# Kernel tuning notes

Measured on AMD Instinct MI355X. Metric: run time of the kernel, lower is better.

The kernel has to match this reference:

```python
import jax, jax.numpy as jnp
import numpy as np

HEADS = 16
EPS = 1e-6


def _rmsnorm(x, gamma):
    # x: [..., head_dim]
    inv = jax.lax.rsqrt(jnp.mean(x * x, axis=-1, keepdims=True) + EPS)
    return x * inv * gamma


def setup_inputs() -> dict:
    key = jax.random.key(0)
    ks = jax.random.split(key, 7)
    B, L, Lc, D, CTX = 4, 4096, 1024, 1024, 1024
    hd = D // HEADS
    s = 1.0 / np.sqrt(D)
    return {
        "x": jax.random.normal(ks[0], (B, L, D), jnp.float32),
        "ctx": jax.random.normal(ks[1], (B, Lc, CTX), jnp.float32),
        "Wq": jax.random.normal(ks[2], (D, D), jnp.float32) * s,
        "Wkv": jax.random.normal(ks[3], (CTX, 2 * D), jnp.float32) * s,
        "Wproj": jax.random.normal(ks[4], (D, D), jnp.float32) * s,
        "q_gamma": jnp.ones((hd,), jnp.float32),
        "k_gamma": jnp.ones((hd,), jnp.float32),
    }


def reference(x, ctx, Wq, Wkv, Wproj, q_gamma, k_gamma):
    B, L, D = x.shape
    Lc = ctx.shape[1]
    H = HEADS
    hd = D // H
    # projections
    q = (x @ Wq).reshape(B, L, H, hd).transpose(0, 2, 1, 3)        # [B,H,L,hd]
    kv = (ctx @ Wkv).reshape(B, Lc, 2, H, hd).transpose(2, 0, 3, 1, 4)
    k, v = kv[0], kv[1]                                            # [B,H,Lc,hd]
    # per-head QK RMSNorm
    q = _rmsnorm(q, q_gamma)
    k = _rmsnorm(k, k_gamma)
    scale = 1.0 / np.sqrt(hd)
    attn = jnp.einsum("bhld,bhmd->bhlm", q, k) * scale             # [B,H,L,Lc]
    attn = jax.nn.softmax(attn, axis=-1)
    out = jnp.einsum("bhlm,bhmd->bhld", attn, v)                   # [B,H,L,hd]
    out = out.transpose(0, 2, 1, 3).reshape(B, L, D)
    return out @ Wproj
```

## Files before the change

### kernel.cpp

```cpp
#include <hip/hip_runtime.h>

typedef __bf16 bf16x8 __attribute__((ext_vector_type(8)));
typedef __bf16 bf16x4 __attribute__((ext_vector_type(4)));
typedef float f32x4 __attribute__((ext_vector_type(4)));

__device__ __forceinline__ void gl_lds16(const void* g, void* l) {
  __builtin_amdgcn_global_load_lds(
      (const __attribute__((address_space(1))) unsigned int*)g,
      (__attribute__((address_space(3))) unsigned int*)l, 16, 0, 0);
}

__global__ __launch_bounds__(256) void conv_bf16_kernel(
    const float* __restrict__ in, __bf16* __restrict__ out, int n4) {
  int i = blockIdx.x * 256 + threadIdx.x;
  if (i < n4) {
    float4 v = ((const float4*)in)[i];
    bf16x4 o;
    o[0] = (__bf16)v.x; o[1] = (__bf16)v.y; o[2] = (__bf16)v.z; o[3] = (__bf16)v.w;
    *(bf16x4*)(out + (size_t)i * 4) = o;
  }
}

__global__ __launch_bounds__(256) void tconv_kernel(
    const float* __restrict__ W, __bf16* __restrict__ Wt, int R, int C) {
  __shared__ float t[32][33];
  int c0 = blockIdx.x * 32, r0 = blockIdx.y * 32;
  int tx = threadIdx.x, ty = threadIdx.y;
#pragma unroll
  for (int i = 0; i < 4; ++i)
    t[ty + i * 8][tx] = W[(size_t)(r0 + ty + i * 8) * C + c0 + tx];
  __syncthreads();
#pragma unroll
  for (int i = 0; i < 4; ++i)
    Wt[(size_t)(c0 + ty + i * 8) * R + r0 + tx] = (__bf16)t[tx][ty + i * 8];
}

template <int NORM, int OUTF32>
__global__ __launch_bounds__(256) void gemm_kernel(
    const __bf16* __restrict__ A, const __bf16* __restrict__ Bt,
    void* __restrict__ Cout, void* __restrict__ Cout2,
    int M, int N, int K, const float* __restrict__ gamma) {
  __shared__ alignas(16) __bf16 Alds[2][128 * 32];
  __shared__ alignas(16) __bf16 Blds[2][128 * 32];
  const int tid = threadIdx.x;
  const int w = tid >> 6, l = tid & 63;
  const int lg = l & 15, lh = l >> 4;
  const int wr = w >> 1, wc = w & 1;

  const int nbx = gridDim.x;
  const int lid = blockIdx.y * nbx + blockIdx.x;
  const int cpx = (nbx * gridDim.y) >> 3;
  const int swz = (lid & 7) * cpx + (lid >> 3);
  const int brow = (swz / nbx) * 128, bcol = (swz % nbx) * 128;

  const f32x4 zero = {0.f, 0.f, 0.f, 0.f};
  f32x4 acc[4][4];
#pragma unroll
  for (int m = 0; m < 4; ++m)
#pragma unroll
    for (int n = 0; n < 4; ++n) acc[m][n] = zero;

  auto STAGE = [&](int buf, int k0) {
#pragma unroll
    for (int j = 0; j < 2; ++j) {
      int c = j * 256 + w * 64 + l;
      gl_lds16(A + (size_t)(brow + (c >> 2)) * K + k0 + (c & 3) * 8,
               (char*)Alds[buf] + (j * 256 + w * 64) * 16);
      gl_lds16(Bt + (size_t)(bcol + (c >> 2)) * K + k0 + (c & 3) * 8,
               (char*)Blds[buf] + (j * 256 + w * 64) * 16);
    }
  };

  STAGE(0, 0);
  __syncthreads();
  for (int k0 = 0; k0 < K; k0 += 32) {
    int cur = (k0 >> 5) & 1;
    if (k0 + 32 < K) STAGE(cur ^ 1, k0 + 32);
    bf16x8 af[4], bfr[4];
#pragma unroll
    for (int m = 0; m < 4; ++m)
      af[m] = *(const bf16x8*)(Alds[cur] + (wr * 64 + m * 16 + lg) * 32 + lh * 8);
#pragma unroll
    for (int n = 0; n < 4; ++n)
      bfr[n] = *(const bf16x8*)(Blds[cur] + (wc * 64 + n * 16 + lg) * 32 + lh * 8);
#pragma unroll
    for (int m = 0; m < 4; ++m)
#pragma unroll
      for (int n = 0; n < 4; ++n)
        acc[m][n] = __builtin_amdgcn_mfma_f32_16x16x32_bf16(af[m], bfr[n], acc[m][n], 0, 0, 0);
    __syncthreads();
  }

  const int col64 = bcol + wc * 64;
  if (NORM == 1 || (NORM == 2 && col64 < 1024)) {
    float gm[4];
#pragma unroll
    for (int n = 0; n < 4; ++n) gm[n] = gamma[n * 16 + lg];
#pragma unroll
    for (int m = 0; m < 4; ++m) {
#pragma unroll
      for (int i = 0; i < 4; ++i) {
        float ss = 0.f;
#pragma unroll
        for (int n = 0; n < 4; ++n) ss += acc[m][n][i] * acc[m][n][i];
        ss += __shfl_xor(ss, 1);
        ss += __shfl_xor(ss, 2);
        ss += __shfl_xor(ss, 4);
        ss += __shfl_xor(ss, 8);
        float inv = rsqrtf(ss * (1.0f / 64.0f) + 1e-6f);
#pragma unroll
        for (int n = 0; n < 4; ++n) acc[m][n][i] *= inv * gm[n];
      }
    }
  }

  if (NORM == 2) {
    if (col64 < 1024) {
#pragma unroll
      for (int m = 0; m < 4; ++m)
#pragma unroll
        for (int n = 0; n < 4; ++n)
#pragma unroll
          for (int i = 0; i < 4; ++i) {
            size_t idx = (size_t)(brow + wr * 64 + m * 16 + lh * 4 + i) * 1024 +
                         col64 + n * 16 + lg;
            ((__bf16*)Cout)[idx] = (__bf16)acc[m][n][i];
          }
    } else {
#pragma unroll
      for (int m = 0; m < 4; ++m) {
        int row = brow + wr * 64 + m * 16 + lh * 4;
        int bb = row >> 10, kv0 = row & 1023;
        int g = kv0 & 31;
        int pos = (kv0 & ~31) + ((g & 15) >> 2) * 8 + (g >> 4) * 4;
#pragma unroll
        for (int n = 0; n < 4; ++n) {
          int col = col64 + n * 16 + lg - 1024;
          bf16x4 v;
#pragma unroll
          for (int i = 0; i < 4; ++i) v[i] = (__bf16)acc[m][n][i];
          *(bf16x4*)((__bf16*)Cout2 + ((size_t)(bb * 1024 + col)) * 1024 + pos) = v;
        }
      }
    }
    return;
  }

#pragma unroll
  for (int m = 0; m < 4; ++m)
#pragma unroll
    for (int n = 0; n < 4; ++n)
#pragma unroll
      for (int i = 0; i < 4; ++i) {
        size_t idx = (size_t)(brow + wr * 64 + m * 16 + lh * 4 + i) * N +
                     bcol + wc * 64 + n * 16 + lg;
        if (OUTF32) ((float*)Cout)[idx] = acc[m][n][i];
        else ((__bf16*)Cout)[idx] = (__bf16)acc[m][n][i];
      }
}

__global__ __launch_bounds__(512) void flash_kernel(
    const __bf16* __restrict__ Qb, const __bf16* __restrict__ Kb,
    const __bf16* __restrict__ Vt, __bf16* __restrict__ Ob) {
  const int orig = blockIdx.x;
  const int wgid = (orig & 7) * 128 + (orig >> 3);
  const int qt = wgid & 15, h = (wgid >> 4) & 15, b = wgid >> 8;
  const int tid = threadIdx.x;
  const int w = tid >> 6, l = tid & 63, lg = l & 15, lh = l >> 4;
  __shared__ alignas(16) char lds[65536];

  const int qrow0 = b * 4096 + qt * 256 + w * 32;
  bf16x8 qfr[2][2];
#pragma unroll
  for (int mff = 0; mff < 2; ++mff)
#pragma unroll
    for (int dc = 0; dc < 2; ++dc)
      qfr[mff][dc] = *(const bf16x8*)(Qb + (size_t)(qrow0 + mff * 16 + lg) * 1024 +
                                      h * 64 + dc * 32 + lh * 8);

  const char* Kg = (const char*)Kb + (size_t)b * 2097152 + h * 128;
  const char* Vg = (const char*)Vt + (size_t)(b * 16 + h) * 64 * 2048;

  const int o16 = tid * 16;
  const int op = o16 ^ (((o16 >> 7) & 7) << 4);
  const int srow = op >> 7, scb = op & 127;

  auto STAGE = [&](int buf, int kt) {
    gl_lds16(Kg + (size_t)(kt * 64 + srow) * 2048 + scb, lds + buf * 8192 + w * 1024);
    gl_lds16(Vg + (size_t)srow * 2048 + kt * 128 + scb, lds + 32768 + buf * 8192 + w * 1024);
  };

  const int swzl = (lg & 7) << 4;
  const int off0 = lg * 128 + ((lh * 16) ^ swzl);
  const int off1 = lg * 128 + ((64 + lh * 16) ^ swzl);

  const f32x4 zero = {0.f, 0.f, 0.f, 0.f};
  f32x4 o_[4][2];
  float m_[2], lp_[2];
#pragma unroll
  for (int df = 0; df < 4; ++df)
#pragma unroll
    for (int qf = 0; qf < 2; ++qf) o_[df][qf] = zero;
  m_[0] = m_[1] = -1e30f;
  lp_[0] = lp_[1] = 0.f;

  const float C = 0.18033688f;
  const float DT = 44.361f;

  auto COMPUTE = [&](const char* Kc, const char* Vc) {
    f32x4 st[4][2];
#pragma unroll
    for (int kvf = 0; kvf < 4; ++kvf)
#pragma unroll
      for (int mff = 0; mff < 2; ++mff) st[kvf][mff] = zero;
    __builtin_amdgcn_s_setprio(1);
#pragma unroll
    for (int dc = 0; dc < 2; ++dc)
#pragma unroll
      for (int kvf = 0; kvf < 4; ++kvf) {
        bf16x8 kf = *(const bf16x8*)(Kc + (dc ? off1 : off0) + kvf * 2048);
#pragma unroll
        for (int mff = 0; mff < 2; ++mff)
          st[kvf][mff] = __builtin_amdgcn_mfma_f32_16x16x32_bf16(kf, qfr[mff][dc], st[kvf][mff], 0, 0, 0);
      }
    __builtin_amdgcn_s_setprio(0);

    float pmax[2];
#pragma unroll
    for (int qf = 0; qf < 2; ++qf) {
      float ma[4];
#pragma unroll
      for (int i = 0; i < 4; ++i)
        ma[i] = fmaxf(fmaxf(st[0][qf][i], st[1][qf][i]),
                      fmaxf(st[2][qf][i], st[3][qf][i]));
      float t = fmaxf(fmaxf(ma[0], ma[1]), fmaxf(ma[2], ma[3]));
      t = fmaxf(t, __shfl_xor(t, 16));
      t = fmaxf(t, __shfl_xor(t, 32));
      pmax[qf] = t;
    }

    int need = (pmax[0] - m_[0] > DT) || (pmax[1] - m_[1] > DT);
    if (__any(need)) {
#pragma unroll
      for (int qf = 0; qf < 2; ++qf) {
        float nm = fmaxf(m_[qf], pmax[qf]);
        float r = __builtin_amdgcn_exp2f((m_[qf] - nm) * C);
        m_[qf] = nm;
        lp_[qf] *= r;
#pragma unroll
        for (int df = 0; df < 4; ++df)
#pragma unroll
          for (int i = 0; i < 4; ++i) o_[df][qf][i] *= r;
      }
    }

    bf16x4 pb[4][2];
#pragma unroll
    for (int qf = 0; qf < 2; ++qf) {
      float rs = 0.f;
      float mc = -m_[qf] * C;
#pragma unroll
      for (int kvf = 0; kvf < 4; ++kvf) {
#pragma unroll
        for (int i = 0; i < 4; ++i) {
          float p = __builtin_amdgcn_exp2f(fmaf(st[kvf][qf][i], C, mc));
          pb[kvf][qf][i] = (__bf16)p;
          rs += p;
        }
      }
      lp_[qf] += rs;
    }

    __builtin_amdgcn_s_setprio(1);
#pragma unroll
    for (int p = 0; p < 2; ++p) {
      union { bf16x4 hv[2]; bf16x8 v; } pc[2];
#pragma unroll
      for (int qf = 0; qf < 2; ++qf) {
        pc[qf].hv[0] = pb[2 * p][qf];
        pc[qf].hv[1] = pb[2 * p + 1][qf];
      }
#pragma unroll
      for (int df = 0; df < 4; ++df) {
        bf16x8 vv = *(const bf16x8*)(Vc + (p ? off1 : off0) + df * 2048);
#pragma unroll
        for (int qf = 0; qf < 2; ++qf)
          o_[df][qf] = __builtin_amdgcn_mfma_f32_16x16x32_bf16(vv, pc[qf].v, o_[df][qf], 0, 0, 0);
      }
    }
    __builtin_amdgcn_s_setprio(0);
  };

  STAGE(0, 0);
  STAGE(1, 1);
  __syncthreads();
#pragma unroll 2
  for (int it = 0; it < 8; ++it) {
    const int pb_ = (it & 1) * 2;
    if (it < 7) {
      STAGE(pb_ ^ 2, 2 * it + 2);
      STAGE((pb_ ^ 2) + 1, 2 * it + 3);
    }
    COMPUTE(lds + pb_ * 8192, lds + 32768 + pb_ * 8192);
    COMPUTE(lds + (pb_ + 1) * 8192, lds + 32768 + (pb_ + 1) * 8192);
    asm volatile("s_waitcnt vmcnt(0)" ::: "memory");
    __syncthreads();
  }

#pragma unroll
  for (int qf = 0; qf < 2; ++qf) {
    float ls = lp_[qf];
    ls += __shfl_xor(ls, 16);
    ls += __shfl_xor(ls, 32);
    float inv = 1.f / ls;
    size_t qrow = (size_t)(qrow0 + qf * 16 + lg) * 1024 + h * 64;
#pragma unroll
    for (int df = 0; df < 4; ++df) {
      bf16x4 ov;
#pragma unroll
      for (int i = 0; i < 4; ++i) ov[i] = (__bf16)(o_[df][qf][i] * inv);
      *(bf16x4*)(Ob + qrow + df * 16 + lh * 4) = ov;
    }
  }
}

extern "C" void kernel_launch(void* const* d_in, const int* in_sizes, int n_in,
                              void* d_out, int out_size, void* d_ws, size_t ws_size,
                              hipStream_t stream) {
  const float* x     = (const float*)d_in[0];
  const float* ctx   = (const float*)d_in[1];
  const float* Wq    = (const float*)d_in[2];
  const float* Wkv   = (const float*)d_in[3];
  const float* Wproj = (const float*)d_in[4];
  const float* qg    = (const float*)d_in[5];
  const float* kg    = (const float*)d_in[6];
  float* out = (float*)d_out;

  char* ws = (char*)d_ws;
  __bf16* xb   = (__bf16*)(ws);
  __bf16* cb   = (__bf16*)(ws + (size_t)32 * 1048576);
  __bf16* Wqt  = (__bf16*)(ws + (size_t)40 * 1048576);
  __bf16* Wkvt = (__bf16*)(ws + (size_t)42 * 1048576);
  __bf16* Wpt  = (__bf16*)(ws + (size_t)46 * 1048576);
  __bf16* Qb   = (__bf16*)(ws + (size_t)48 * 1048576);
  __bf16* Kb   = (__bf16*)(ws + (size_t)80 * 1048576);
  __bf16* Vt   = (__bf16*)(ws + (size_t)88 * 1048576);
  __bf16* Ob   = xb;

  conv_bf16_kernel<<<16384, 256, 0, stream>>>(x, xb, 4194304);
  conv_bf16_kernel<<<4096, 256, 0, stream>>>(ctx, cb, 1048576);
  tconv_kernel<<<dim3(32, 32), dim3(32, 8), 0, stream>>>(Wq, Wqt, 1024, 1024);
  tconv_kernel<<<dim3(64, 32), dim3(32, 8), 0, stream>>>(Wkv, Wkvt, 1024, 2048);
  tconv_kernel<<<dim3(32, 32), dim3(32, 8), 0, stream>>>(Wproj, Wpt, 1024, 1024);

  gemm_kernel<1, 0><<<dim3(8, 128), 256, 0, stream>>>(xb, Wqt, Qb, nullptr, 16384, 1024, 1024, qg);
  gemm_kernel<2, 0><<<dim3(16, 32), 256, 0, stream>>>(cb, Wkvt, Kb, Vt, 4096, 2048, 1024, kg);
  flash_kernel<<<1024, 512, 0, stream>>>(Qb, Kb, Vt, Ob);
  gemm_kernel<0, 1><<<dim3(8, 128), 256, 0, stream>>>(Ob, Wpt, out, nullptr, 16384, 1024, 1024, nullptr);
}
```

Measured before the change: 258.0 us.

## Split attention step into QK, softmax and PV phases and interleave two tiles

The per-tile COMPUTE lambda is split into separate QK^T, softmax and PV stages. Both K tiles' QK^T MFMAs are now issued before either softmax runs, so exp and VALU work can overlap the matrix units. The cross-lane max shuffles now run only when a rescale is actually needed, and P values are written straight into bf16x8 MFMA operands. A launch bound of (512,4) is also added, which caps registers per thread even though the 64KB LDS per block limits residency anyway, so it risks spills given the larger live state from holding two score tiles.

```diff
diff --git a/kernel.cpp b/kernel.cpp
--- a/kernel.cpp
+++ b/kernel.cpp
@@ -159,7 +159,7 @@
       }
 }
 
-__global__ __launch_bounds__(512) void flash_kernel(
+__global__ __launch_bounds__(512, 4) void flash_kernel(
     const __bf16* __restrict__ Qb, const __bf16* __restrict__ Kb,
     const __bf16* __restrict__ Vt, __bf16* __restrict__ Ob) {
   const int orig = blockIdx.x;
@@ -207,24 +207,26 @@
   const float C = 0.18033688f;
   const float DT = 44.361f;
 
-  auto COMPUTE = [&](const char* Kc, const char* Vc) {
-    f32x4 st[4][2];
-#pragma unroll
-    for (int kvf = 0; kvf < 4; ++kvf)
-#pragma unroll
-      for (int mff = 0; mff < 2; ++mff) st[kvf][mff] = zero;
+  auto QKT = [&](const char* Kc, f32x4 (&st)[4][2]) {
     __builtin_amdgcn_s_setprio(1);
 #pragma unroll
-    for (int dc = 0; dc < 2; ++dc)
-#pragma unroll
-      for (int kvf = 0; kvf < 4; ++kvf) {
-        bf16x8 kf = *(const bf16x8*)(Kc + (dc ? off1 : off0) + kvf * 2048);
-#pragma unroll
-        for (int mff = 0; mff < 2; ++mff)
-          st[kvf][mff] = __builtin_amdgcn_mfma_f32_16x16x32_bf16(kf, qfr[mff][dc], st[kvf][mff], 0, 0, 0);
-      }
+    for (int kvf = 0; kvf < 4; ++kvf) {
+      bf16x8 kf = *(const bf16x8*)(Kc + off0 + kvf * 2048);
+#pragma unroll
+      for (int mff = 0; mff < 2; ++mff)
+        st[kvf][mff] = __builtin_amdgcn_mfma_f32_16x16x32_bf16(kf, qfr[mff][0], zero, 0, 0, 0);
+    }
+#pragma unroll
+    for (int kvf = 0; kvf < 4; ++kvf) {
+      bf16x8 kf = *(const bf16x8*)(Kc + off1 + kvf * 2048);
+#pragma unroll
+      for (int mff = 0; mff < 2; ++mff)
+        st[kvf][mff] = __builtin_amdgcn_mfma_f32_16x16x32_bf16(kf, qfr[mff][1], st[kvf][mff], 0, 0, 0);
+    }
     __builtin_amdgcn_s_setprio(0);
-
+  };
+
+  auto SM = [&](f32x4 (&st)[4][2], bf16x8 (&pw)[2][2]) {
     float pmax[2];
 #pragma unroll
     for (int qf = 0; qf < 2; ++qf) {
@@ -233,17 +235,16 @@
       for (int i = 0; i < 4; ++i)
         ma[i] = fmaxf(fmaxf(st[0][qf][i], st[1][qf][i]),
                       fmaxf(st[2][qf][i], st[3][qf][i]));
-      float t = fmaxf(fmaxf(ma[0], ma[1]), fmaxf(ma[2], ma[3]));
-      t = fmaxf(t, __shfl_xor(t, 16));
-      t = fmaxf(t, __shfl_xor(t, 32));
-      pmax[qf] = t;
-    }
-
+      pmax[qf] = fmaxf(fmaxf(ma[0], ma[1]), fmaxf(ma[2], ma[3]));
+    }
     int need = (pmax[0] - m_[0] > DT) || (pmax[1] - m_[1] > DT);
     if (__any(need)) {
 #pragma unroll
       for (int qf = 0; qf < 2; ++qf) {
-        float nm = fmaxf(m_[qf], pmax[qf]);
+        float t = pmax[qf];
+        t = fmaxf(t, __shfl_xor(t, 16));
+        t = fmaxf(t, __shfl_xor(t, 32));
+        float nm = fmaxf(m_[qf], t);
         float r = __builtin_amdgcn_exp2f((m_[qf] - nm) * C);
         m_[qf] = nm;
         lp_[qf] *= r;
@@ -253,8 +254,6 @@
           for (int i = 0; i < 4; ++i) o_[df][qf][i] *= r;
       }
     }
-
-    bf16x4 pb[4][2];
 #pragma unroll
     for (int qf = 0; qf < 2; ++qf) {
       float rs = 0.f;
@@ -264,30 +263,25 @@
 #pragma unroll
         for (int i = 0; i < 4; ++i) {
           float p = __builtin_amdgcn_exp2f(fmaf(st[kvf][qf][i], C, mc));
-          pb[kvf][qf][i] = (__bf16)p;
+          pw[kvf >> 1][qf][(kvf & 1) * 4 + i] = (__bf16)p;
           rs += p;
         }
       }
       lp_[qf] += rs;
     }
-
+  };
+
+  auto PV = [&](const char* Vc, bf16x8 (&pw)[2][2]) {
     __builtin_amdgcn_s_setprio(1);
 #pragma unroll
-    for (int p = 0; p < 2; ++p) {
-      union { bf16x4 hv[2]; bf16x8 v; } pc[2];
-#pragma unroll
-      for (int qf = 0; qf < 2; ++qf) {
-        pc[qf].hv[0] = pb[2 * p][qf];
-        pc[qf].hv[1] = pb[2 * p + 1][qf];
-      }
+    for (int p = 0; p < 2; ++p)
 #pragma unroll
       for (int df = 0; df < 4; ++df) {
         bf16x8 vv = *(const bf16x8*)(Vc + (p ? off1 : off0) + df * 2048);
 #pragma unroll
         for (int qf = 0; qf < 2; ++qf)
-          o_[df][qf] = __builtin_amdgcn_mfma_f32_16x16x32_bf16(vv, pc[qf].v, o_[df][qf], 0, 0, 0);
-      }
-    }
+          o_[df][qf] = __builtin_amdgcn_mfma_f32_16x16x32_bf16(vv, pw[p][qf], o_[df][qf], 0, 0, 0);
+      }
     __builtin_amdgcn_s_setprio(0);
   };
 
@@ -301,8 +295,14 @@
       STAGE(pb_ ^ 2, 2 * it + 2);
       STAGE((pb_ ^ 2) + 1, 2 * it + 3);
     }
-    COMPUTE(lds + pb_ * 8192, lds + 32768 + pb_ * 8192);
-    COMPUTE(lds + (pb_ + 1) * 8192, lds + 32768 + (pb_ + 1) * 8192);
+    f32x4 stA[4][2], stB[4][2];
+    bf16x8 pwA[2][2], pwB[2][2];
+    QKT(lds + pb_ * 8192, stA);
+    QKT(lds + (pb_ + 1) * 8192, stB);
+    SM(stA, pwA);
+    PV(lds + 32768 + pb_ * 8192, pwA);
+    SM(stB, pwB);
+    PV(lds + 32768 + (pb_ + 1) * 8192, pwB);
     asm volatile("s_waitcnt vmcnt(0)" ::: "memory");
     __syncthreads();
   }
```

Measured after the change: 295.9 us. 14.7% more time.
